# Kernel optimization log

Measured on AMD Instinct MI355X. Metric: run time of the kernel, lower is better.

Reference implementation:

```python
import jax, jax.numpy as jnp
import numpy as np

N, T, D, W, H = 2, 1024, 256, 128, 8
HD = D // H


def setup_inputs() -> dict:
    key = jax.random.key(0)
    ks = jax.random.split(key, 5)
    s = 0.05
    return {
        "inputs": jax.random.normal(ks[0], (N, T, D), jnp.float32),
        "in_proj_w": jax.random.normal(ks[1], (3 * D, D), jnp.float32) * s,
        "in_proj_b": jax.random.normal(ks[2], (3 * D,), jnp.float32) * s,
        "out_w": jax.random.normal(ks[3], (D, D), jnp.float32) * s,
        "out_b": jax.random.normal(ks[4], (D,), jnp.float32) * s,
    }


def reference(inputs, in_proj_w, in_proj_b, out_w, out_b):
    n, t, d = inputs.shape
    # Window with stride=1, lpad='steady': pad W-1 zeros on the left, T_out = T_in
    x = jnp.pad(inputs, ((0, 0), (W - 1, 0), (0, 0)))
    idx = jnp.arange(t)[:, None] + jnp.arange(W)[None, :]  # [T, W]
    windows = x[:, idx]                                    # [N, T, W, D]
    w = windows.reshape(n * t, W, d)
    q = w[:, -1]                                           # [NT, D] (last window element)
    # Faithful to torch: windows.transpose(1,2).reshape(-1, W, D) on contiguous data
    kv = jnp.swapaxes(w, 1, 2).reshape(n * t, W, d)        # [NT, W, D]
    Wq, Wk, Wv = in_proj_w[:d], in_proj_w[d:2 * d], in_proj_w[2 * d:]
    bq, bk, bv = in_proj_b[:d], in_proj_b[d:2 * d], in_proj_b[2 * d:]
    qh = (q @ Wq.T + bq).reshape(n * t, H, HD)             # [NT, H, HD]
    kh = (kv @ Wk.T + bk).reshape(n * t, W, H, HD)
    vh = (kv @ Wv.T + bv).reshape(n * t, W, H, HD)
    scores = jnp.einsum('nhd,nwhd->nhw', qh, kh) / np.float32(np.sqrt(HD))
    # causal warmup mask: disallow key slot j when j < W-1-t (the zero-padded positions)
    tvec = jnp.arange(t)
    mask = jnp.arange(W)[None, :] < (W - 1 - tvec)[:, None]  # [T, W], True = masked
    mask = jnp.broadcast_to(mask[None], (n, t, W)).reshape(n * t, 1, W)
    scores = jnp.where(mask, -jnp.inf, scores)
    attn = jax.nn.softmax(scores, axis=-1)
    out = jnp.einsum('nhw,nwhd->nhd', attn, vh).reshape(n * t, d)
    out = out @ out_w.T + out_b
    return out.reshape(n, t, 1, d)
```

## Files before the change

### kernel.cpp

```cpp
#include <hip/hip_runtime.h>
#include <math.h>

#define NTOK 2048
#define TT   1024
constexpr float SCL = 0.17677669529663687f;

#define OFF_WQT 0
#define OFF_WKT 65536
#define OFF_WVT 131072
#define OFF_OWT 196608
#define OFF_RQ  262144
#define OFF_SB  4456448
#define OFF_CTX 4472832

#define GLOAD_LDS16(g, l)                                                      \
    __builtin_amdgcn_global_load_lds(                                          \
        (const __attribute__((address_space(1))) unsigned int*)(g),            \
        (__attribute__((address_space(3))) unsigned int*)(l), 16, 0, 0)

__global__ __launch_bounds__(256) void k0_transpose(const float* __restrict__ ipw,
                                                    const float* __restrict__ ow,
                                                    float* __restrict__ ws) {
    __shared__ float tile[32][33];
    int bx = blockIdx.x;
    int mat = bx >> 6, tl = bx & 63;
    int tr0 = (tl >> 3) << 5, tc0 = (tl & 7) << 5;
    const float* src;
    float* dst;
    if (mat == 3) { src = ow;             dst = ws + OFF_OWT; }
    else          { src = ipw + mat*65536; dst = ws + OFF_WQT + mat*65536; }
    int c = threadIdx.x & 31, r0 = threadIdx.x >> 5;
    #pragma unroll
    for (int k = 0; k < 4; k++) {
        int r = r0 + k*8;
        tile[r][c] = src[(tr0 + r)*256 + tc0 + c];
    }
    __syncthreads();
    #pragma unroll
    for (int k = 0; k < 4; k++) {
        int r = r0 + k*8;
        dst[(tc0 + r)*256 + tr0 + c] = tile[c][r];
    }
}

__global__ __launch_bounds__(512) void k1_qrq(const float* __restrict__ x,
                                              const float* __restrict__ ipw,
                                              const float* __restrict__ ipb,
                                              float* __restrict__ ws) {
    __shared__ float x8[2048];
    __shared__ float qpart[4096];
    __shared__ float qh[2048];
    extern __shared__ float rqt[];
    const float* wqT = ws + OFF_WQT;
    const float* wk  = ipw + 65536;
    float* rqw = ws + OFF_RQ;
    float* sbw = ws + OFF_SB;
    int tid = threadIdx.x;
    long i0 = (long)blockIdx.x * 8;

    ((float4*)x8)[tid] = ((const float4*)(x + i0*256))[tid];
    __syncthreads();

    int c = tid & 255, half = tid >> 8;
    {
        float qa[8];
        #pragma unroll
        for (int ii = 0; ii < 8; ii++) qa[ii] = 0.f;
        int cc0 = half*128;
        #pragma unroll 8
        for (int cc = cc0; cc < cc0 + 128; cc++) {
            float w = wqT[cc*256 + c];
            #pragma unroll
            for (int ii = 0; ii < 8; ii++) qa[ii] += x8[ii*256 + cc]*w;
        }
        #pragma unroll
        for (int ii = 0; ii < 8; ii++) qpart[(half*8 + ii)*256 + c] = qa[ii];
    }
    __syncthreads();
    if (tid < 256) {
        float b = ipb[tid];
        #pragma unroll
        for (int ii = 0; ii < 8; ii++)
            qh[ii*256 + tid] = qpart[ii*256 + tid] + qpart[(8 + ii)*256 + tid] + b;
    }
    __syncthreads();
    {
        int k = tid & 255, hh = tid >> 8;
        int s = k & 127, par = k >> 7;
        for (int h = hh*4; h < hh*4 + 4; h++) {
            float ra[8];
            #pragma unroll
            for (int ii = 0; ii < 8; ii++) ra[ii] = 0.f;
            #pragma unroll 8
            for (int hd = 0; hd < 32; hd++) {
                float w = wk[(h*32 + hd)*256 + k];
                #pragma unroll
                for (int ii = 0; ii < 8; ii++) ra[ii] += qh[ii*256 + h*32 + hd]*w;
            }
            int h2p = h*2 + par;
            #pragma unroll
            for (int ii = 0; ii < 8; ii++)
                rqt[ii*2112 + h2p*132 + s] = ra[ii]*SCL;
        }
    }
    __syncthreads();
    {
        float4* dst = (float4*)(rqw + i0*2048);
        #pragma unroll
        for (int it = 0; it < 8; it++) {
            int f = it*512 + tid;
            int s = (f & 511) >> 2, q = f & 3;
            int base = it*2112 + s;
            float4 v;
            v.x = rqt[base + (4*q + 0)*132];
            v.y = rqt[base + (4*q + 1)*132];
            v.z = rqt[base + (4*q + 2)*132];
            v.w = rqt[base + (4*q + 3)*132];
            dst[f] = v;
        }
    }
    if (tid < 64) {
        int ii = tid >> 3, h = tid & 7;
        float s = 0.f;
        #pragma unroll 8
        for (int hd = 0; hd < 32; hd++) s += qh[ii*256 + h*32 + hd]*ipb[256 + h*32 + hd];
        sbw[(i0 + ii)*8 + h] = s*SCL;
    }
}

__global__ __launch_bounds__(1024) void k2_attn(const float* __restrict__ x,
                                                float* __restrict__ ws) {
    extern __shared__ float sm[];
    float* xw   = sm;
    float* rq2  = sm + 33280;
    float* scp  = sm + 33280 + 2048;
    float* attn = rq2;
    const float* rqw = ws + OFF_RQ;
    const float* sbw = ws + OFF_SB;
    float* ctxw = ws + OFF_CTX;
    int tid = threadIdx.x;
    int i = blockIdx.x;
    int t = i & (TT - 1);
    int w = tid >> 6, lane = tid & 63;

    {
        #pragma unroll
        for (int it = 0; it < 8; it++) {
            int r = it*16 + w;
            int ts = t - 127 + r;
            float* lrow = xw + r*260;
            if (ts >= 0) {
                const float* g = x + (long)(i - 127 + r)*256 + lane*4;
                GLOAD_LDS16(g, lrow);
            } else {
                float4 z = {0.f, 0.f, 0.f, 0.f};
                *(float4*)(lrow + lane*4) = z;
            }
        }
        if (w < 8) {
            const float* g = rqw + (long)i*2048 + w*256 + lane*4;
            GLOAD_LDS16(g, rq2 + w*256);
        }
    }
    __syncthreads();

    {
        int jj2 = lane;
        int q = w >> 2, hh4 = w & 3;
        float a00=0.f,a01=0.f,a10=0.f,a11=0.f;
        const float4* rq4 = (const float4*)rq2;
        int s0 = q*32;
        #pragma unroll 4
        for (int s = s0; s < s0 + 32; s++) {
            float4 xv = *(const float4*)&xw[s*260 + 4*jj2];
            float4 r0 = rq4[s*4 + hh4];
            a00 += r0.x*xv.x + r0.y*xv.y;  a01 += r0.x*xv.z + r0.y*xv.w;
            a10 += r0.z*xv.x + r0.w*xv.y;  a11 += r0.z*xv.z + r0.w*xv.w;
        }
        float2* sc2 = (float2*)scp;
        float2 v0 = {a00, a01}; sc2[q*512 + (2*hh4+0)*64 + jj2] = v0;
        float2 v1 = {a10, a11}; sc2[q*512 + (2*hh4+1)*64 + jj2] = v1;
    }
    __syncthreads();

    if (w < 8) {
        int h = w, l = lane;
        float sb = sbw[i*8 + h];
        float s1 = sb, s2 = sb;
        #pragma unroll
        for (int q = 0; q < 4; q++) {
            s1 += scp[q*1024 + h*128 + l];
            s2 += scp[q*1024 + h*128 + l + 64];
        }
        int lim = 127 - t;
        bool m1 = l < lim, m2 = (l + 64) < lim;
        if (m1) s1 = -1e30f;
        if (m2) s2 = -1e30f;
        float m = fmaxf(s1, s2);
        #pragma unroll
        for (int d = 1; d < 64; d <<= 1) m = fmaxf(m, __shfl_xor(m, d, 64));
        float e1 = m1 ? 0.f : __expf(s1 - m);
        float e2 = m2 ? 0.f : __expf(s2 - m);
        float sum = e1 + e2;
        #pragma unroll
        for (int d = 1; d < 64; d <<= 1) sum += __shfl_xor(sum, d, 64);
        float r = 1.0f / sum;
        attn[l*8 + h] = e1*r;
        attn[(l + 64)*8 + h] = e2*r;
    }
    __syncthreads();

    {
        int sC = tid & 127, jq = tid >> 7;
        float cac[16];
        #pragma unroll
        for (int c = 0; c < 16; c++) cac[c] = 0.f;
        #pragma unroll 4
        for (int j = jq*16; j < jq*16 + 16; j++) {
            float2 x2 = *(const float2*)&xw[sC*260 + 2*j];
            float4 a0 = *(const float4*)&attn[j*8];
            float4 a1 = *(const float4*)&attn[j*8 + 4];
            cac[0]  += a0.x*x2.x; cac[1]  += a0.y*x2.x; cac[2]  += a0.z*x2.x; cac[3]  += a0.w*x2.x;
            cac[4]  += a1.x*x2.x; cac[5]  += a1.y*x2.x; cac[6]  += a1.z*x2.x; cac[7]  += a1.w*x2.x;
            cac[8]  += a0.x*x2.y; cac[9]  += a0.y*x2.y; cac[10] += a0.z*x2.y; cac[11] += a0.w*x2.y;
            cac[12] += a1.x*x2.y; cac[13] += a1.y*x2.y; cac[14] += a1.z*x2.y; cac[15] += a1.w*x2.y;
        }
        __syncthreads();
        #pragma unroll
        for (int c = 0; c < 16; c++) xw[c*1024 + tid] = cac[c];
    }
    __syncthreads();

    if (tid < 256) {
        int k = tid, p = k >> 7;
        float v[8];
        #pragma unroll
        for (int h = 0; h < 8; h++) v[h] = 0.f;
        #pragma unroll
        for (int jq = 0; jq < 8; jq++) {
            int thr = jq*128 + (k & 127);
            #pragma unroll
            for (int h = 0; h < 8; h++) v[h] += xw[(p*8 + h)*1024 + thr];
        }
        float4* dst = (float4*)(ctxw + (long)i*2048 + k*8);
        float4 o0 = {v[0], v[1], v[2], v[3]};
        float4 o1 = {v[4], v[5], v[6], v[7]};
        dst[0] = o0; dst[1] = o1;
    }
}

__global__ __launch_bounds__(512) void k3_proj(const float* __restrict__ ipb,
                                               const float* __restrict__ ob,
                                               float* __restrict__ ws,
                                               float* __restrict__ out) {
    extern __shared__ float sm[];
    float* ctx8T  = sm;
    float* oppart = sm + 8192;
    float* op     = sm + 8192 + 2048;
    const float* wvT  = ws + OFF_WVT;
    const float* owT  = ws + OFF_OWT;
    const float* ctxw = ws + OFF_CTX;
    int tid = threadIdx.x;
    long i0 = (long)blockIdx.x * 4;

    {
        const float* src = ctxw + i0*2048;
        #pragma unroll
        for (int it = 0; it < 4; it++) {
            int kh8 = it*512 + tid;
            float4 v;
            #pragma unroll
            for (int ii = 0; ii < 4; ii++)
                (&v.x)[ii] = src[ii*2048 + kh8];
            *(float4*)&ctx8T[kh8*4] = v;
        }
    }
    __syncthreads();

    int c = tid & 255, kh = tid >> 8;
    {
        int h = c >> 5;
        float acc[4];
        #pragma unroll
        for (int ii = 0; ii < 4; ii++) acc[ii] = 0.f;
        #pragma unroll 8
        for (int k = kh*128; k < kh*128 + 128; k++) {
            float w = wvT[k*256 + c];
            float4 cv = *(const float4*)&ctx8T[(k*8 + h)*4];
            acc[0] += w*cv.x; acc[1] += w*cv.y; acc[2] += w*cv.z; acc[3] += w*cv.w;
        }
        #pragma unroll
        for (int ii = 0; ii < 4; ii++) oppart[(kh*4 + ii)*256 + c] = acc[ii];
    }
    __syncthreads();
    if (tid < 256) {
        float b = ipb[512 + tid];
        #pragma unroll
        for (int ii = 0; ii < 4; ii++)
            op[ii*256 + tid] = oppart[ii*256 + tid] + oppart[(4 + ii)*256 + tid] + b;
    }
    __syncthreads();
    {
        float acc[4];
        #pragma unroll
        for (int ii = 0; ii < 4; ii++) acc[ii] = 0.f;
        #pragma unroll 8
        for (int cc = kh*128; cc < kh*128 + 128; cc++) {
            float w = owT[cc*256 + c];
            #pragma unroll
            for (int ii = 0; ii < 4; ii++) acc[ii] += w*op[ii*256 + cc];
        }
        #pragma unroll
        for (int ii = 0; ii < 4; ii++) oppart[(kh*4 + ii)*256 + c] = acc[ii];
    }
    __syncthreads();
    if (tid < 256) {
        float b = ob[tid];
        #pragma unroll
        for (int ii = 0; ii < 4; ii++)
            out[(i0 + ii)*256 + tid] = oppart[ii*256 + tid] + oppart[(4 + ii)*256 + tid] + b;
    }
}

extern "C" void kernel_launch(void* const* d_in, const int* in_sizes, int n_in,
                              void* d_out, int out_size, void* d_ws, size_t ws_size,
                              hipStream_t stream) {
    const float* x   = (const float*)d_in[0];
    const float* ipw = (const float*)d_in[1];
    const float* ipb = (const float*)d_in[2];
    const float* ow  = (const float*)d_in[3];
    const float* ob  = (const float*)d_in[4];
    float* out = (float*)d_out;
    float* ws  = (float*)d_ws;

    (void)in_sizes; (void)n_in; (void)out_size; (void)ws_size;

    hipFuncSetAttribute(reinterpret_cast<const void*>(k1_qrq),
                        hipFuncAttributeMaxDynamicSharedMemorySize, 67584);
    hipFuncSetAttribute(reinterpret_cast<const void*>(k2_attn),
                        hipFuncAttributeMaxDynamicSharedMemorySize, 157696);
    hipFuncSetAttribute(reinterpret_cast<const void*>(k3_proj),
                        hipFuncAttributeMaxDynamicSharedMemorySize, 45056);

    hipLaunchKernelGGL(k0_transpose, dim3(256),  dim3(256),  0,      stream, ipw, ow, ws);
    hipLaunchKernelGGL(k1_qrq,       dim3(256),  dim3(512),  67584,  stream, x, ipw, ipb, ws);
    hipLaunchKernelGGL(k2_attn,      dim3(2048), dim3(1024), 157696, stream, x, ws);
    hipLaunchKernelGGL(k3_proj,      dim3(512),  dim3(512),  45056,  stream, ipb, ob, ws, out);
}
```

Baseline: 171.0 us.

## Halve k1 tokens per block and restructure k2 score loop with LDS atomics

Result: slower. 330.7 us (+93.4%).

```diff
diff --git a/kernel.cpp b/kernel.cpp
--- a/kernel.cpp
+++ b/kernel.cpp
@@ -47,59 +47,59 @@
                                               const float* __restrict__ ipw,
                                               const float* __restrict__ ipb,
                                               float* __restrict__ ws) {
-    __shared__ float x8[2048];
-    __shared__ float qpart[4096];
-    __shared__ float qh[2048];
+    __shared__ float x4s[1024];
+    __shared__ float qpart[2048];
+    __shared__ float qh[1024];
     extern __shared__ float rqt[];
     const float* wqT = ws + OFF_WQT;
     const float* wk  = ipw + 65536;
     float* rqw = ws + OFF_RQ;
     float* sbw = ws + OFF_SB;
     int tid = threadIdx.x;
-    long i0 = (long)blockIdx.x * 8;
-
-    ((float4*)x8)[tid] = ((const float4*)(x + i0*256))[tid];
+    long i0 = (long)blockIdx.x * 4;
+
+    if (tid < 256) ((float4*)x4s)[tid] = ((const float4*)(x + i0*256))[tid];
     __syncthreads();
 
     int c = tid & 255, half = tid >> 8;
     {
-        float qa[8];
-        #pragma unroll
-        for (int ii = 0; ii < 8; ii++) qa[ii] = 0.f;
+        float qa[4];
+        #pragma unroll
+        for (int ii = 0; ii < 4; ii++) qa[ii] = 0.f;
         int cc0 = half*128;
         #pragma unroll 8
         for (int cc = cc0; cc < cc0 + 128; cc++) {
             float w = wqT[cc*256 + c];
             #pragma unroll
-            for (int ii = 0; ii < 8; ii++) qa[ii] += x8[ii*256 + cc]*w;
-        }
-        #pragma unroll
-        for (int ii = 0; ii < 8; ii++) qpart[(half*8 + ii)*256 + c] = qa[ii];
+            for (int ii = 0; ii < 4; ii++) qa[ii] += x4s[ii*256 + cc]*w;
+        }
+        #pragma unroll
+        for (int ii = 0; ii < 4; ii++) qpart[(half*4 + ii)*256 + c] = qa[ii];
     }
     __syncthreads();
     if (tid < 256) {
         float b = ipb[tid];
         #pragma unroll
-        for (int ii = 0; ii < 8; ii++)
-            qh[ii*256 + tid] = qpart[ii*256 + tid] + qpart[(8 + ii)*256 + tid] + b;
+        for (int ii = 0; ii < 4; ii++)
+            qh[ii*256 + tid] = qpart[ii*256 + tid] + qpart[(4 + ii)*256 + tid] + b;
     }
     __syncthreads();
     {
         int k = tid & 255, hh = tid >> 8;
         int s = k & 127, par = k >> 7;
         for (int h = hh*4; h < hh*4 + 4; h++) {
-            float ra[8];
-            #pragma unroll
-            for (int ii = 0; ii < 8; ii++) ra[ii] = 0.f;
+            float ra[4];
+            #pragma unroll
+            for (int ii = 0; ii < 4; ii++) ra[ii] = 0.f;
             #pragma unroll 8
             for (int hd = 0; hd < 32; hd++) {
                 float w = wk[(h*32 + hd)*256 + k];
                 #pragma unroll
-                for (int ii = 0; ii < 8; ii++) ra[ii] += qh[ii*256 + h*32 + hd]*w;
+                for (int ii = 0; ii < 4; ii++) ra[ii] += qh[ii*256 + h*32 + hd]*w;
             }
             int h2p = h*2 + par;
             #pragma unroll
-            for (int ii = 0; ii < 8; ii++)
+            for (int ii = 0; ii < 4; ii++)
                 rqt[ii*2112 + h2p*132 + s] = ra[ii]*SCL;
         }
     }
@@ -107,7 +107,7 @@
     {
         float4* dst = (float4*)(rqw + i0*2048);
         #pragma unroll
-        for (int it = 0; it < 8; it++) {
+        for (int it = 0; it < 4; it++) {
             int f = it*512 + tid;
             int s = (f & 511) >> 2, q = f & 3;
             int base = it*2112 + s;
@@ -119,7 +119,7 @@
             dst[f] = v;
         }
     }
-    if (tid < 64) {
+    if (tid < 32) {
         int ii = tid >> 3, h = tid & 7;
         float s = 0.f;
         #pragma unroll 8
@@ -144,6 +144,8 @@
     int w = tid >> 6, lane = tid & 63;
 
     {
+        float4 z = {0.f, 0.f, 0.f, 0.f};
+        ((float4*)scp)[tid] = z;
         #pragma unroll
         for (int it = 0; it < 8; it++) {
             int r = it*16 + w;
@@ -153,7 +155,6 @@
                 const float* g = x + (long)(i - 127 + r)*256 + lane*4;
                 GLOAD_LDS16(g, lrow);
             } else {
-                float4 z = {0.f, 0.f, 0.f, 0.f};
                 *(float4*)(lrow + lane*4) = z;
             }
         }
@@ -165,21 +166,34 @@
     __syncthreads();
 
     {
-        int jj2 = lane;
-        int q = w >> 2, hh4 = w & 3;
-        float a00=0.f,a01=0.f,a10=0.f,a11=0.f;
+        int q = w >> 2, sh = w & 3;
+        float a[16];
+        #pragma unroll
+        for (int m = 0; m < 16; m++) a[m] = 0.f;
         const float4* rq4 = (const float4*)rq2;
-        int s0 = q*32;
-        #pragma unroll 4
-        for (int s = s0; s < s0 + 32; s++) {
-            float4 xv = *(const float4*)&xw[s*260 + 4*jj2];
-            float4 r0 = rq4[s*4 + hh4];
-            a00 += r0.x*xv.x + r0.y*xv.y;  a01 += r0.x*xv.z + r0.y*xv.w;
-            a10 += r0.z*xv.x + r0.w*xv.y;  a11 += r0.z*xv.z + r0.w*xv.w;
-        }
-        float2* sc2 = (float2*)scp;
-        float2 v0 = {a00, a01}; sc2[q*512 + (2*hh4+0)*64 + jj2] = v0;
-        float2 v1 = {a10, a11}; sc2[q*512 + (2*hh4+1)*64 + jj2] = v1;
+        int s0 = q*32 + sh*8;
+        #pragma unroll
+        for (int s = s0; s < s0 + 8; s++) {
+            float4 xv = *(const float4*)&xw[s*260 + 4*lane];
+            float4 r0 = rq4[s*4 + 0];
+            float4 r1 = rq4[s*4 + 1];
+            float4 r2 = rq4[s*4 + 2];
+            float4 r3 = rq4[s*4 + 3];
+            a[0]  += r0.x*xv.x + r0.y*xv.y;  a[1]  += r0.x*xv.z + r0.y*xv.w;
+            a[2]  += r0.z*xv.x + r0.w*xv.y;  a[3]  += r0.z*xv.z + r0.w*xv.w;
+            a[4]  += r1.x*xv.x + r1.y*xv.y;  a[5]  += r1.x*xv.z + r1.y*xv.w;
+            a[6]  += r1.z*xv.x + r1.w*xv.y;  a[7]  += r1.z*xv.z + r1.w*xv.w;
+            a[8]  += r2.x*xv.x + r2.y*xv.y;  a[9]  += r2.x*xv.z + r2.y*xv.w;
+            a[10] += r2.z*xv.x + r2.w*xv.y;  a[11] += r2.z*xv.z + r2.w*xv.w;
+            a[12] += r3.x*xv.x + r3.y*xv.y;  a[13] += r3.x*xv.z + r3.y*xv.w;
+            a[14] += r3.z*xv.x + r3.w*xv.y;  a[15] += r3.z*xv.z + r3.w*xv.w;
+        }
+        int j0 = 2*lane;
+        #pragma unroll
+        for (int h = 0; h < 8; h++) {
+            atomicAdd(&scp[q*1024 + h*128 + j0],     a[2*h]);
+            atomicAdd(&scp[q*1024 + h*128 + j0 + 1], a[2*h + 1]);
+        }
     }
     __syncthreads();
 
@@ -336,14 +350,14 @@
     (void)in_sizes; (void)n_in; (void)out_size; (void)ws_size;
 
     hipFuncSetAttribute(reinterpret_cast<const void*>(k1_qrq),
-                        hipFuncAttributeMaxDynamicSharedMemorySize, 67584);
+                        hipFuncAttributeMaxDynamicSharedMemorySize, 33792);
     hipFuncSetAttribute(reinterpret_cast<const void*>(k2_attn),
                         hipFuncAttributeMaxDynamicSharedMemorySize, 157696);
     hipFuncSetAttribute(reinterpret_cast<const void*>(k3_proj),
                         hipFuncAttributeMaxDynamicSharedMemorySize, 45056);
 
     hipLaunchKernelGGL(k0_transpose, dim3(256),  dim3(256),  0,      stream, ipw, ow, ws);
-    hipLaunchKernelGGL(k1_qrq,       dim3(256),  dim3(512),  67584,  stream, x, ipw, ipb, ws);
+    hipLaunchKernelGGL(k1_qrq,       dim3(512),  dim3(512),  33792,  stream, x, ipw, ipb, ws);
     hipLaunchKernelGGL(k2_attn,      dim3(2048), dim3(1024), 157696, stream, x, ws);
     hipLaunchKernelGGL(k3_proj,      dim3(512),  dim3(512),  45056,  stream, ipb, ob, ws, out);
 }
```
